# Optimization experiments

Measured on AMD Instinct MI355X. Metric: run time of the kernel, lower is better.

The kernel has to match this reference:

```python
import jax, jax.numpy as jnp
import numpy as np

N_NODES = 100000
N_EDGES = 1600000
IN_CH = 128
HEADS = 4
HID = 32
OUT_CH = 128
NEG_SLOPE = 0.2


def setup_inputs() -> dict:
    key = jax.random.key(0)
    ks = jax.random.split(key, 7)
    sc = 1.0 / np.sqrt(IN_CH)
    return {
        "x": jax.random.normal(ks[0], (N_NODES, IN_CH), dtype=jnp.float32),
        "edge_index": jax.random.randint(ks[1], (2, N_EDGES), 0, N_NODES, dtype=jnp.int32),
        "W": jax.random.normal(ks[2], (IN_CH, HEADS * HID), dtype=jnp.float32) * sc,
        "att_src": jax.random.normal(ks[3], (HEADS, HID), dtype=jnp.float32) * sc,
        "att_dst": jax.random.normal(ks[4], (HEADS, HID), dtype=jnp.float32) * sc,
        "lin_w": jax.random.normal(ks[5], (HEADS * HID, OUT_CH), dtype=jnp.float32) * (1.0 / np.sqrt(HEADS * HID)),
        "lin_b": jax.random.normal(ks[6], (OUT_CH,), dtype=jnp.float32) * 0.01,
    }


def reference(x, edge_index, W, att_src, att_dst, lin_w, lin_b):
    N = x.shape[0]
    src, dst = edge_index[0], edge_index[1]
    # node-wise linear transform -> [N, H, C]
    h = (x @ W).reshape(N, HEADS, HID)
    # per-node attention logit components [N, H]
    a_src = jnp.einsum("nhc,hc->nh", h, att_src)
    a_dst = jnp.einsum("nhc,hc->nh", h, att_dst)
    # per-edge logits with LeakyReLU [E, H]
    e = jax.nn.leaky_relu(a_src[src] + a_dst[dst], negative_slope=NEG_SLOPE)
    # segment softmax over destination neighborhoods
    m = jax.ops.segment_max(e, dst, num_segments=N)
    ex = jnp.exp(e - m[dst])
    s = jax.ops.segment_sum(ex, dst, num_segments=N)
    alpha = ex / (s[dst] + 1e-16)
    # weighted scatter-sum of source features [N, H, C] -> concat heads
    msg = h[src] * alpha[:, :, None]
    out = jax.ops.segment_sum(msg, dst, num_segments=N).reshape(N, HEADS * HID)
    # trailing dense + ReLU
    return jax.nn.relu(out @ lin_w + lin_b)
```

## Files before the change

kernel.cpp:

```cpp
#include <hip/hip_runtime.h>
#include <hip/hip_fp16.h>

#define NB   256
#define NBLK 256
#define BSH  9

typedef _Float16 f16;
typedef _Float16 half8 __attribute__((ext_vector_type(8)));
typedef __fp16 pk16x2 __attribute__((ext_vector_type(2)));
typedef float f32x4 __attribute__((ext_vector_type(4)));

__global__ void k_prep(const float* __restrict__ W, const float* __restrict__ LW,
                       f16* __restrict__ Wt, f16* __restrict__ LWt)
{
    int n = blockIdx.x & 127;
    const float* src = (blockIdx.x < 128) ? W : LW;
    f16* dst = (blockIdx.x < 128) ? Wt : LWt;
    int k = threadIdx.x;
    dst[n * 128 + k] = (f16)src[k * 128 + n];
}

__global__ __launch_bounds__(256) void k_gemm_att(
    const float* __restrict__ A, const f16* __restrict__ Wt,
    const float* __restrict__ att_s, const float* __restrict__ att_d,
    f16* __restrict__ Hh, float* __restrict__ as_out, float* __restrict__ ad_out,
    int M)
{
    __shared__ __align__(16) f16 as_lds[64 * 136];
    int t = threadIdx.x;
    int row0 = blockIdx.x * 64;

    {
        int r = t >> 2, kq = (t & 3) * 32;
        const float* ap = A + (size_t)(row0 + r) * 128 + kq;
        bool valid = (row0 + r) < M;
        pk16x2 hb[16];
#pragma unroll
        for (int j = 0; j < 8; ++j) {
            float4 v = valid ? *(const float4*)(ap + j * 4) : make_float4(0.f, 0.f, 0.f, 0.f);
            hb[2 * j]     = __builtin_amdgcn_cvt_pkrtz(v.x, v.y);
            hb[2 * j + 1] = __builtin_amdgcn_cvt_pkrtz(v.z, v.w);
        }
        f16* dst = as_lds + r * 136 + kq;
#pragma unroll
        for (int j = 0; j < 4; ++j) *(float4*)(dst + j * 8) = ((float4*)hb)[j];
    }
    __syncthreads();

    int w = t >> 6, ln = t & 63;
    int rr = (w & 1) * 32;
    int cc = (w >> 1) * 64;
    int q = ln >> 4, m = ln & 15;

    f32x4 acc[2][4];
#pragma unroll
    for (int i = 0; i < 2; ++i)
#pragma unroll
        for (int j = 0; j < 4; ++j) acc[i][j] = (f32x4){0.f, 0.f, 0.f, 0.f};

    const f16* wp = Wt + (size_t)(cc + m) * 128 + q * 8;
#pragma unroll
    for (int ks = 0; ks < 4; ++ks) {
        int k0 = ks * 32 + q * 8;
        half8 a0 = *(const half8*)(as_lds + (rr + m) * 136 + k0);
        half8 a1 = *(const half8*)(as_lds + (rr + 16 + m) * 136 + k0);
        half8 bf[4];
#pragma unroll
        for (int j = 0; j < 4; ++j)
            bf[j] = *(const half8*)(wp + j * 16 * 128 + ks * 32);
#pragma unroll
        for (int j = 0; j < 4; ++j) {
            acc[0][j] = __builtin_amdgcn_mfma_f32_16x16x32_f16(a0, bf[j], acc[0][j], 0, 0, 0);
            acc[1][j] = __builtin_amdgcn_mfma_f32_16x16x32_f16(a1, bf[j], acc[1][j], 0, 0, 0);
        }
    }
    __syncthreads();
#pragma unroll
    for (int i = 0; i < 2; ++i)
#pragma unroll
        for (int j = 0; j < 4; ++j)
#pragma unroll
            for (int g = 0; g < 4; ++g)
                as_lds[(rr + i * 16 + q * 4 + g) * 136 + cc + j * 16 + m] = (f16)acc[i][j][g];
    __syncthreads();
    {
        int r = t >> 2, cq = (t & 3) * 32;
        if (row0 + r < M) {
            float4 o0 = *(const float4*)(as_lds + r * 136 + cq);
            float4 o1 = *(const float4*)(as_lds + r * 136 + cq + 8);
            float4 o2 = *(const float4*)(as_lds + r * 136 + cq + 16);
            float4 o3 = *(const float4*)(as_lds + r * 136 + cq + 24);
            float4* hp = (float4*)(Hh + (size_t)(row0 + r) * 128 + cq);
            hp[0] = o0; hp[1] = o1; hp[2] = o2; hp[3] = o3;
        }
    }
    {
        int rl = w * 16 + m;
        int head = q;
        float ds = 0.f, dd = 0.f;
#pragma unroll
        for (int ch = 0; ch < 4; ++ch) {
            half8 hv = *(const half8*)(as_lds + rl * 136 + head * 32 + ch * 8);
            float4 s0 = *(const float4*)(att_s + head * 32 + ch * 8);
            float4 s1 = *(const float4*)(att_s + head * 32 + ch * 8 + 4);
            float4 d0 = *(const float4*)(att_d + head * 32 + ch * 8);
            float4 d1 = *(const float4*)(att_d + head * 32 + ch * 8 + 4);
            ds += (float)hv[0] * s0.x + (float)hv[1] * s0.y + (float)hv[2] * s0.z + (float)hv[3] * s0.w
                + (float)hv[4] * s1.x + (float)hv[5] * s1.y + (float)hv[6] * s1.z + (float)hv[7] * s1.w;
            dd += (float)hv[0] * d0.x + (float)hv[1] * d0.y + (float)hv[2] * d0.z + (float)hv[3] * d0.w
                + (float)hv[4] * d1.x + (float)hv[5] * d1.y + (float)hv[6] * d1.z + (float)hv[7] * d1.w;
        }
        if (row0 + rl < M) {
            as_out[(row0 + rl) * 4 + head] = ds;
            ad_out[(row0 + rl) * 4 + head] = dd;
        }
    }
}

__global__ __launch_bounds__(256) void k_gemm_bias_relu(
    const f16* __restrict__ Ah, const f16* __restrict__ LWt,
    const float* __restrict__ bias, float* __restrict__ Out, int M)
{
    __shared__ __align__(16) f16 as_lds[64 * 136];
    int t = threadIdx.x;
    int row0 = blockIdx.x * 64;
    {
        int r = t >> 2, kq = (t & 3) * 32;
        f16* dst = as_lds + r * 136 + kq;
        if (row0 + r < M) {
            const float4* ap = (const float4*)(Ah + (size_t)(row0 + r) * 128 + kq);
#pragma unroll
            for (int j = 0; j < 4; ++j) *(float4*)(dst + j * 8) = ap[j];
        } else {
            float4 z = make_float4(0.f, 0.f, 0.f, 0.f);
#pragma unroll
            for (int j = 0; j < 4; ++j) *(float4*)(dst + j * 8) = z;
        }
    }
    __syncthreads();

    int w = t >> 6, ln = t & 63;
    int rr = (w & 1) * 32;
    int cc = (w >> 1) * 64;
    int q = ln >> 4, m = ln & 15;

    f32x4 acc[2][4];
#pragma unroll
    for (int i = 0; i < 2; ++i)
#pragma unroll
        for (int j = 0; j < 4; ++j) acc[i][j] = (f32x4){0.f, 0.f, 0.f, 0.f};

    const f16* wp = LWt + (size_t)(cc + m) * 128 + q * 8;
#pragma unroll
    for (int ks = 0; ks < 4; ++ks) {
        int k0 = ks * 32 + q * 8;
        half8 a0 = *(const half8*)(as_lds + (rr + m) * 136 + k0);
        half8 a1 = *(const half8*)(as_lds + (rr + 16 + m) * 136 + k0);
        half8 bf[4];
#pragma unroll
        for (int j = 0; j < 4; ++j)
            bf[j] = *(const half8*)(wp + j * 16 * 128 + ks * 32);
#pragma unroll
        for (int j = 0; j < 4; ++j) {
            acc[0][j] = __builtin_amdgcn_mfma_f32_16x16x32_f16(a0, bf[j], acc[0][j], 0, 0, 0);
            acc[1][j] = __builtin_amdgcn_mfma_f32_16x16x32_f16(a1, bf[j], acc[1][j], 0, 0, 0);
        }
    }
    float bv[4];
#pragma unroll
    for (int j = 0; j < 4; ++j) bv[j] = bias[cc + j * 16 + m];
#pragma unroll
    for (int i = 0; i < 2; ++i)
#pragma unroll
        for (int g = 0; g < 4; ++g) {
            int row = row0 + rr + i * 16 + q * 4 + g;
            if (row < M) {
#pragma unroll
                for (int j = 0; j < 4; ++j)
                    Out[(size_t)row * 128 + cc + j * 16 + m] = fmaxf(acc[i][j][g] + bv[j], 0.f);
            }
        }
}


__global__ __launch_bounds__(256) void k_ph_hist(
    const int* __restrict__ dst, int* __restrict__ bh, int E, int chunk)
{
    __shared__ int hist[NB];
    int t = threadIdx.x;
    hist[t] = 0;
    __syncthreads();
    int e0 = blockIdx.x * chunk;
    int e1 = min(e0 + chunk, E);
    for (int e = e0 + t; e < e1; e += 256)
        atomicAdd(&hist[dst[e] >> BSH], 1);
    __syncthreads();
    bh[t * NBLK + blockIdx.x] = hist[t];
}

__global__ __launch_bounds__(1024) void k_ph_scan(int* __restrict__ bh)
{
    __shared__ int sd[1024];
    const int per = (NB * NBLK) / 1024;
    int t = threadIdx.x;
    int base = t * per;
    int loc[per];
    int sum = 0;
#pragma unroll
    for (int j = 0; j < per; ++j) { loc[j] = bh[base + j]; sum += loc[j]; }
    sd[t] = sum;
    __syncthreads();
    for (int o = 1; o < 1024; o <<= 1) {
        int x = (t >= o) ? sd[t - o] : 0;
        __syncthreads();
        sd[t] += x;
        __syncthreads();
    }
    int run = sd[t] - sum;
#pragma unroll
    for (int j = 0; j < per; ++j) { bh[base + j] = run; run += loc[j]; }
}

__global__ __launch_bounds__(256) void k_ph_bin(
    const int* __restrict__ ei, const int* __restrict__ bh,
    int* __restrict__ binned, int E, int chunk)
{
    __shared__ int boff[NB];
    int t = threadIdx.x;
    boff[t] = bh[t * NBLK + blockIdx.x];
    __syncthreads();
    int e0 = blockIdx.x * chunk;
    int e1 = min(e0 + chunk, E);
    for (int e = e0 + t; e < e1; e += 256) {
        int s = ei[e];
        int d = ei[E + e];
        int p = atomicAdd(&boff[d >> BSH], 1);
        binned[p] = s | ((d & ((1 << BSH) - 1)) << 17);
    }
}

__global__ __launch_bounds__(256) void k_ph_csr(
    const int* __restrict__ binned, const int* __restrict__ bh,
    int* __restrict__ csr, int* __restrict__ off, int* __restrict__ deg,
    int N, int E)
{
    __shared__ int cnt[512], loff[512], sd[256];
    int b = blockIdx.x;
    int lo = b << BSH;
    if (lo >= N) return;
    int t = threadIdx.x;
    int seg = bh[b * NBLK];
    int segend = (b + 1 < NB) ? bh[(b + 1) * NBLK] : E;
    int len = segend - seg;
    cnt[t] = 0; cnt[t + 256] = 0;
    __syncthreads();
    for (int i = t; i < len; i += 256)
        atomicAdd(&cnt[(unsigned)binned[seg + i] >> 17], 1);
    __syncthreads();
    int a0 = cnt[2 * t], a1 = cnt[2 * t + 1];
    int s = a0 + a1;
    sd[t] = s;
    __syncthreads();
    for (int o = 1; o < 256; o <<= 1) {
        int x = (t >= o) ? sd[t - o] : 0;
        __syncthreads();
        sd[t] += x;
        __syncthreads();
    }
    int ex = sd[t] - s;
    loff[2 * t] = ex;
    loff[2 * t + 1] = ex + a0;
    int n0 = lo + 2 * t;
    if (n0 < N)     { off[n0] = seg + ex;          deg[n0] = a0; }
    if (n0 + 1 < N) { off[n0 + 1] = seg + ex + a0; deg[n0 + 1] = a1; }
    __syncthreads();
    for (int i = t; i < len; i += 256) {
        int v = binned[seg + i];
        int p = atomicAdd(&loff[(unsigned)v >> 17], 1);
        csr[seg + p] = v & 0x1ffff;
    }
}

__global__ __launch_bounds__(256) void k_gather(
    const __half* __restrict__ Hh, const float* __restrict__ as_,
    const float* __restrict__ ad_, const int* __restrict__ off,
    const int* __restrict__ deg, const int* __restrict__ csr,
    __half* __restrict__ P, int N)
{
    __shared__ __half2 exh[4][4][68];
    __shared__ int src_s[4][64];
    int wid = threadIdx.x >> 6;
    int lane = threadIdx.x & 63;
    int n = blockIdx.x * 4 + wid;
    if (n >= N) return;
    int dg = deg[n];
    int base = off[n];
    float4 adn = *(const float4*)(ad_ + (size_t)n * 4);
    int g = lane >> 4;
    int li = lane & 15;
    int hh = li >> 2;
    float s0 = 0.f, s1 = 0.f, s2 = 0.f, s3 = 0.f;
    float acc[8] = {0.f, 0.f, 0.f, 0.f, 0.f, 0.f, 0.f, 0.f};

    for (int c0 = 0; c0 < dg; c0 += 64) {
        int cnt = min(64, dg - c0);
        {
            int idx = c0 + lane;
            int se = csr[base + min(idx, dg - 1)];
            float4 as = *(const float4*)(as_ + (size_t)se * 4);
            float e0 = as.x + adn.x, e1 = as.y + adn.y;
            float e2 = as.z + adn.z, e3 = as.w + adn.w;
            e0 = fmaxf(e0, 0.2f * e0); e1 = fmaxf(e1, 0.2f * e1);
            e2 = fmaxf(e2, 0.2f * e2); e3 = fmaxf(e3, 0.2f * e3);
            float x0 = __expf(e0), x1 = __expf(e1);
            float x2 = __expf(e2), x3 = __expf(e3);
            if (idx >= dg) { x0 = x1 = x2 = x3 = 0.f; }
            s0 += x0; s1 += x1; s2 += x2; s3 += x3;
            exh[wid][0][lane] = __float2half2_rn(x0);
            exh[wid][1][lane] = __float2half2_rn(x1);
            exh[wid][2][lane] = __float2half2_rn(x2);
            exh[wid][3][lane] = __float2half2_rn(x3);
            src_s[wid][lane] = se;
        }
        __asm__ volatile("s_waitcnt lgkmcnt(0)" ::: "memory");
        int iters = (cnt + 3) >> 2;
        __half2 ah[4];
        ah[0] = ah[1] = ah[2] = ah[3] = __float2half2_rn(0.f);
        for (int ii = 0; ii < iters; ++ii) {
            int j = ii * 4 + g;
            __half2 w2 = exh[wid][hh][j];
            int se = src_s[wid][j];
            float4 raw = *(const float4*)(Hh + (size_t)se * 128 + li * 8);
            __half2* ph = (__half2*)&raw;
            ah[0] = __hfma2(ph[0], w2, ah[0]);
            ah[1] = __hfma2(ph[1], w2, ah[1]);
            ah[2] = __hfma2(ph[2], w2, ah[2]);
            ah[3] = __hfma2(ph[3], w2, ah[3]);
            if ((ii & 7) == 7) {
#pragma unroll
                for (int k = 0; k < 4; ++k) {
                    float2 f = __half22float2(ah[k]);
                    acc[2 * k] += f.x; acc[2 * k + 1] += f.y;
                    ah[k] = __float2half2_rn(0.f);
                }
            }
        }
#pragma unroll
        for (int k = 0; k < 4; ++k) {
            float2 f = __half22float2(ah[k]);
            acc[2 * k] += f.x; acc[2 * k + 1] += f.y;
        }
        __asm__ volatile("s_waitcnt lgkmcnt(0)" ::: "memory");
    }

#pragma unroll
    for (int o = 1; o < 64; o <<= 1) {
        s0 += __shfl_xor(s0, o);
        s1 += __shfl_xor(s1, o);
        s2 += __shfl_xor(s2, o);
        s3 += __shfl_xor(s3, o);
    }
#pragma unroll
    for (int o = 16; o < 64; o <<= 1)
#pragma unroll
        for (int c = 0; c < 8; ++c) acc[c] += __shfl_xor(acc[c], o);

    float sh = (hh == 0) ? s0 : (hh == 1) ? s1 : (hh == 2) ? s2 : s3;
    float inv = 1.f / (sh + 1e-16f);
    if (g == 0) {
        __half2 o4[4];
#pragma unroll
        for (int k = 0; k < 4; ++k)
            o4[k] = __float22half2_rn(make_float2(acc[2 * k] * inv, acc[2 * k + 1] * inv));
        *(float4*)(P + (size_t)n * 128 + li * 8) = *(float4*)o4;
    }
}


extern "C" void kernel_launch(void* const* d_in, const int* in_sizes, int n_in,
                              void* d_out, int out_size, void* d_ws, size_t ws_size,
                              hipStream_t stream)
{
    const float* x     = (const float*)d_in[0];
    const int*   ei    = (const int*)d_in[1];
    const float* W     = (const float*)d_in[2];
    const float* att_s = (const float*)d_in[3];
    const float* att_d = (const float*)d_in[4];
    const float* lin_w = (const float*)d_in[5];
    const float* lin_b = (const float*)d_in[6];
    float* out = (float*)d_out;
    int N = in_sizes[0] / 128;
    int E = in_sizes[1] / 2;

    char* p = (char*)d_ws;
    auto alloc = [&](size_t bytes) { char* r = p; p += (bytes + 255) & ~(size_t)255; return r; };
    f16*    Hh   = (f16*)alloc((size_t)N * 128 * 2);
    f16*    P    = (f16*)alloc((size_t)N * 128 * 2);
    f16*    Wt   = (f16*)alloc(128 * 128 * 2);
    f16*    LWt  = (f16*)alloc(128 * 128 * 2);
    float*  AS   = (float*)alloc((size_t)N * 4 * 4);
    float*  AD   = (float*)alloc((size_t)N * 4 * 4);
    int*    deg  = (int*)alloc((size_t)N * 4);
    int*    off  = (int*)alloc((size_t)N * 4);
    int*    csr  = (int*)alloc((size_t)E * 4);
    int*    binned = (int*)alloc((size_t)E * 4);
    int*    bh   = (int*)alloc((size_t)NB * NBLK * 4);

    int chunk = (E + NBLK - 1) / NBLK;
    int mb = (N + 63) / 64;
    k_prep<<<256, 128, 0, stream>>>(W, lin_w, Wt, LWt);
    k_gemm_att<<<mb, 256, 0, stream>>>(x, Wt, att_s, att_d, Hh, AS, AD, N);
    k_ph_hist<<<NBLK, 256, 0, stream>>>(ei + E, bh, E, chunk);
    k_ph_scan<<<1, 1024, 0, stream>>>(bh);
    k_ph_bin<<<NBLK, 256, 0, stream>>>(ei, bh, binned, E, chunk);
    k_ph_csr<<<NB, 256, 0, stream>>>(binned, bh, csr, off, deg, N, E);
    k_gather<<<(N + 3) / 4, 256, 0, stream>>>((const __half*)Hh, AS, AD, off, deg, csr, (__half*)P, N);
    k_gemm_bias_relu<<<mb, 256, 0, stream>>>(P, LWt, lin_b, out, N);
}
```

Baseline: 303.9 us.

## Fuse neighbor aggregation with output GEMM through shared memory

The gather-aggregate kernel and the trailing dense+bias+ReLU GEMM are merged into one kernel. Each block of four waves aggregates 64 destination nodes, 16 per wave, into an LDS tile, then runs the MFMA GEMM on that tile directly. This removes the global round trip of the intermediate P buffer and one kernel launch. The edge weight and source index are also packed into one int2 LDS entry. The cost is 16x fewer blocks with a serial per-wave node loop, so occupancy and load balance over uneven degrees get worse.

```diff
diff --git a/kernel.cpp b/kernel.cpp
--- a/kernel.cpp
+++ b/kernel.cpp
@@ -117,71 +117,6 @@
     }
 }
 
-__global__ __launch_bounds__(256) void k_gemm_bias_relu(
-    const f16* __restrict__ Ah, const f16* __restrict__ LWt,
-    const float* __restrict__ bias, float* __restrict__ Out, int M)
-{
-    __shared__ __align__(16) f16 as_lds[64 * 136];
-    int t = threadIdx.x;
-    int row0 = blockIdx.x * 64;
-    {
-        int r = t >> 2, kq = (t & 3) * 32;
-        f16* dst = as_lds + r * 136 + kq;
-        if (row0 + r < M) {
-            const float4* ap = (const float4*)(Ah + (size_t)(row0 + r) * 128 + kq);
-#pragma unroll
-            for (int j = 0; j < 4; ++j) *(float4*)(dst + j * 8) = ap[j];
-        } else {
-            float4 z = make_float4(0.f, 0.f, 0.f, 0.f);
-#pragma unroll
-            for (int j = 0; j < 4; ++j) *(float4*)(dst + j * 8) = z;
-        }
-    }
-    __syncthreads();
-
-    int w = t >> 6, ln = t & 63;
-    int rr = (w & 1) * 32;
-    int cc = (w >> 1) * 64;
-    int q = ln >> 4, m = ln & 15;
-
-    f32x4 acc[2][4];
-#pragma unroll
-    for (int i = 0; i < 2; ++i)
-#pragma unroll
-        for (int j = 0; j < 4; ++j) acc[i][j] = (f32x4){0.f, 0.f, 0.f, 0.f};
-
-    const f16* wp = LWt + (size_t)(cc + m) * 128 + q * 8;
-#pragma unroll
-    for (int ks = 0; ks < 4; ++ks) {
-        int k0 = ks * 32 + q * 8;
-        half8 a0 = *(const half8*)(as_lds + (rr + m) * 136 + k0);
-        half8 a1 = *(const half8*)(as_lds + (rr + 16 + m) * 136 + k0);
-        half8 bf[4];
-#pragma unroll
-        for (int j = 0; j < 4; ++j)
-            bf[j] = *(const half8*)(wp + j * 16 * 128 + ks * 32);
-#pragma unroll
-        for (int j = 0; j < 4; ++j) {
-            acc[0][j] = __builtin_amdgcn_mfma_f32_16x16x32_f16(a0, bf[j], acc[0][j], 0, 0, 0);
-            acc[1][j] = __builtin_amdgcn_mfma_f32_16x16x32_f16(a1, bf[j], acc[1][j], 0, 0, 0);
-        }
-    }
-    float bv[4];
-#pragma unroll
-    for (int j = 0; j < 4; ++j) bv[j] = bias[cc + j * 16 + m];
-#pragma unroll
-    for (int i = 0; i < 2; ++i)
-#pragma unroll
-        for (int g = 0; g < 4; ++g) {
-            int row = row0 + rr + i * 16 + q * 4 + g;
-            if (row < M) {
-#pragma unroll
-                for (int j = 0; j < 4; ++j)
-                    Out[(size_t)row * 128 + cc + j * 16 + m] = fmaxf(acc[i][j][g] + bv[j], 0.f);
-            }
-        }
-}
-
 
 __global__ __launch_bounds__(256) void k_ph_hist(
     const int* __restrict__ dst, int* __restrict__ bh, int E, int chunk)
@@ -281,99 +216,149 @@
     }
 }
 
-__global__ __launch_bounds__(256) void k_gather(
+__global__ __launch_bounds__(256) void k_gather_gemm(
     const __half* __restrict__ Hh, const float* __restrict__ as_,
     const float* __restrict__ ad_, const int* __restrict__ off,
     const int* __restrict__ deg, const int* __restrict__ csr,
-    __half* __restrict__ P, int N)
-{
-    __shared__ __half2 exh[4][4][68];
-    __shared__ int src_s[4][64];
-    int wid = threadIdx.x >> 6;
-    int lane = threadIdx.x & 63;
-    int n = blockIdx.x * 4 + wid;
-    if (n >= N) return;
-    int dg = deg[n];
-    int base = off[n];
-    float4 adn = *(const float4*)(ad_ + (size_t)n * 4);
+    const f16* __restrict__ LWt, const float* __restrict__ bias,
+    float* __restrict__ Out, int N)
+{
+    __shared__ __align__(16) f16 p_lds[64 * 136];
+    __shared__ int2 ews[4][4][68];
+    int t = threadIdx.x;
+    int w = t >> 6, lane = t & 63;
+    int row0 = blockIdx.x * 64;
+
     int g = lane >> 4;
     int li = lane & 15;
     int hh = li >> 2;
-    float s0 = 0.f, s1 = 0.f, s2 = 0.f, s3 = 0.f;
-    float acc[8] = {0.f, 0.f, 0.f, 0.f, 0.f, 0.f, 0.f, 0.f};
-
-    for (int c0 = 0; c0 < dg; c0 += 64) {
-        int cnt = min(64, dg - c0);
-        {
-            int idx = c0 + lane;
-            int se = csr[base + min(idx, dg - 1)];
-            float4 as = *(const float4*)(as_ + (size_t)se * 4);
-            float e0 = as.x + adn.x, e1 = as.y + adn.y;
-            float e2 = as.z + adn.z, e3 = as.w + adn.w;
-            e0 = fmaxf(e0, 0.2f * e0); e1 = fmaxf(e1, 0.2f * e1);
-            e2 = fmaxf(e2, 0.2f * e2); e3 = fmaxf(e3, 0.2f * e3);
-            float x0 = __expf(e0), x1 = __expf(e1);
-            float x2 = __expf(e2), x3 = __expf(e3);
-            if (idx >= dg) { x0 = x1 = x2 = x3 = 0.f; }
-            s0 += x0; s1 += x1; s2 += x2; s3 += x3;
-            exh[wid][0][lane] = __float2half2_rn(x0);
-            exh[wid][1][lane] = __float2half2_rn(x1);
-            exh[wid][2][lane] = __float2half2_rn(x2);
-            exh[wid][3][lane] = __float2half2_rn(x3);
-            src_s[wid][lane] = se;
-        }
-        __asm__ volatile("s_waitcnt lgkmcnt(0)" ::: "memory");
-        int iters = (cnt + 3) >> 2;
-        __half2 ah[4];
-        ah[0] = ah[1] = ah[2] = ah[3] = __float2half2_rn(0.f);
-        for (int ii = 0; ii < iters; ++ii) {
-            int j = ii * 4 + g;
-            __half2 w2 = exh[wid][hh][j];
-            int se = src_s[wid][j];
-            float4 raw = *(const float4*)(Hh + (size_t)se * 128 + li * 8);
-            __half2* ph = (__half2*)&raw;
-            ah[0] = __hfma2(ph[0], w2, ah[0]);
-            ah[1] = __hfma2(ph[1], w2, ah[1]);
-            ah[2] = __hfma2(ph[2], w2, ah[2]);
-            ah[3] = __hfma2(ph[3], w2, ah[3]);
-            if ((ii & 7) == 7) {
-#pragma unroll
-                for (int k = 0; k < 4; ++k) {
-                    float2 f = __half22float2(ah[k]);
-                    acc[2 * k] += f.x; acc[2 * k + 1] += f.y;
-                    ah[k] = __float2half2_rn(0.f);
+
+    for (int nl = 0; nl < 16; ++nl) {
+        int ln = w * 16 + nl;
+        int n = row0 + ln;
+        if (n >= N) break;
+        int dg = deg[n];
+        int base = off[n];
+        float4 adn = *(const float4*)(ad_ + (size_t)n * 4);
+        float s0 = 0.f, s1 = 0.f, s2 = 0.f, s3 = 0.f;
+        float acc[8] = {0.f, 0.f, 0.f, 0.f, 0.f, 0.f, 0.f, 0.f};
+
+        for (int c0 = 0; c0 < dg; c0 += 64) {
+            int cnt = min(64, dg - c0);
+            {
+                int idx = c0 + lane;
+                int se = csr[base + min(idx, dg - 1)];
+                float4 as = *(const float4*)(as_ + (size_t)se * 4);
+                float e0 = as.x + adn.x, e1 = as.y + adn.y;
+                float e2 = as.z + adn.z, e3 = as.w + adn.w;
+                e0 = fmaxf(e0, 0.2f * e0); e1 = fmaxf(e1, 0.2f * e1);
+                e2 = fmaxf(e2, 0.2f * e2); e3 = fmaxf(e3, 0.2f * e3);
+                float x0 = __expf(e0), x1 = __expf(e1);
+                float x2 = __expf(e2), x3 = __expf(e3);
+                if (idx >= dg) { x0 = x1 = x2 = x3 = 0.f; }
+                s0 += x0; s1 += x1; s2 += x2; s3 += x3;
+                __half2 w0 = __float2half2_rn(x0), w1 = __float2half2_rn(x1);
+                __half2 w2h = __float2half2_rn(x2), w3 = __float2half2_rn(x3);
+                ews[w][0][lane] = make_int2(*(int*)&w0, se);
+                ews[w][1][lane] = make_int2(*(int*)&w1, se);
+                ews[w][2][lane] = make_int2(*(int*)&w2h, se);
+                ews[w][3][lane] = make_int2(*(int*)&w3, se);
+            }
+            __asm__ volatile("s_waitcnt lgkmcnt(0)" ::: "memory");
+            int iters = (cnt + 3) >> 2;
+            __half2 ah[4];
+            ah[0] = ah[1] = ah[2] = ah[3] = __float2half2_rn(0.f);
+            for (int ii = 0; ii < iters; ++ii) {
+                int j = ii * 4 + g;
+                int2 e = ews[w][hh][j];
+                __half2 w2 = *(__half2*)&e.x;
+                float4 raw = *(const float4*)(Hh + (size_t)e.y * 128 + li * 8);
+                __half2* ph = (__half2*)&raw;
+                ah[0] = __hfma2(ph[0], w2, ah[0]);
+                ah[1] = __hfma2(ph[1], w2, ah[1]);
+                ah[2] = __hfma2(ph[2], w2, ah[2]);
+                ah[3] = __hfma2(ph[3], w2, ah[3]);
+                if ((ii & 7) == 7) {
+#pragma unroll
+                    for (int k = 0; k < 4; ++k) {
+                        float2 f = __half22float2(ah[k]);
+                        acc[2 * k] += f.x; acc[2 * k + 1] += f.y;
+                        ah[k] = __float2half2_rn(0.f);
+                    }
                 }
             }
-        }
-#pragma unroll
-        for (int k = 0; k < 4; ++k) {
-            float2 f = __half22float2(ah[k]);
-            acc[2 * k] += f.x; acc[2 * k + 1] += f.y;
-        }
-        __asm__ volatile("s_waitcnt lgkmcnt(0)" ::: "memory");
-    }
-
-#pragma unroll
-    for (int o = 1; o < 64; o <<= 1) {
-        s0 += __shfl_xor(s0, o);
-        s1 += __shfl_xor(s1, o);
-        s2 += __shfl_xor(s2, o);
-        s3 += __shfl_xor(s3, o);
-    }
-#pragma unroll
-    for (int o = 16; o < 64; o <<= 1)
-#pragma unroll
-        for (int c = 0; c < 8; ++c) acc[c] += __shfl_xor(acc[c], o);
-
-    float sh = (hh == 0) ? s0 : (hh == 1) ? s1 : (hh == 2) ? s2 : s3;
-    float inv = 1.f / (sh + 1e-16f);
-    if (g == 0) {
-        __half2 o4[4];
-#pragma unroll
-        for (int k = 0; k < 4; ++k)
-            o4[k] = __float22half2_rn(make_float2(acc[2 * k] * inv, acc[2 * k + 1] * inv));
-        *(float4*)(P + (size_t)n * 128 + li * 8) = *(float4*)o4;
-    }
+#pragma unroll
+            for (int k = 0; k < 4; ++k) {
+                float2 f = __half22float2(ah[k]);
+                acc[2 * k] += f.x; acc[2 * k + 1] += f.y;
+            }
+            __asm__ volatile("s_waitcnt lgkmcnt(0)" ::: "memory");
+        }
+
+#pragma unroll
+        for (int o = 1; o < 64; o <<= 1) {
+            s0 += __shfl_xor(s0, o);
+            s1 += __shfl_xor(s1, o);
+            s2 += __shfl_xor(s2, o);
+            s3 += __shfl_xor(s3, o);
+        }
+#pragma unroll
+        for (int o = 16; o < 64; o <<= 1)
+#pragma unroll
+            for (int c = 0; c < 8; ++c) acc[c] += __shfl_xor(acc[c], o);
+
+        float sh = (hh == 0) ? s0 : (hh == 1) ? s1 : (hh == 2) ? s2 : s3;
+        float inv = 1.f / (sh + 1e-16f);
+        if (g == 0) {
+            pk16x2 o4[4];
+#pragma unroll
+            for (int k = 0; k < 4; ++k)
+                o4[k] = __builtin_amdgcn_cvt_pkrtz(acc[2 * k] * inv, acc[2 * k + 1] * inv);
+            *(float4*)(p_lds + ln * 136 + li * 8) = *(float4*)o4;
+        }
+    }
+    __syncthreads();
+
+    int rr = (w & 1) * 32;
+    int cc = (w >> 1) * 64;
+    int q = lane >> 4, m = lane & 15;
+
+    f32x4 gacc[2][4];
+#pragma unroll
+    for (int i = 0; i < 2; ++i)
+#pragma unroll
+        for (int j = 0; j < 4; ++j) gacc[i][j] = (f32x4){0.f, 0.f, 0.f, 0.f};
+
+    const f16* wp = LWt + (size_t)(cc + m) * 128 + q * 8;
+#pragma unroll
+    for (int ks = 0; ks < 4; ++ks) {
+        int k0 = ks * 32 + q * 8;
+        half8 a0 = *(const half8*)(p_lds + (rr + m) * 136 + k0);
+        half8 a1 = *(const half8*)(p_lds + (rr + 16 + m) * 136 + k0);
+        half8 bf[4];
+#pragma unroll
+        for (int j = 0; j < 4; ++j)
+            bf[j] = *(const half8*)(wp + j * 16 * 128 + ks * 32);
+#pragma unroll
+        for (int j = 0; j < 4; ++j) {
+            gacc[0][j] = __builtin_amdgcn_mfma_f32_16x16x32_f16(a0, bf[j], gacc[0][j], 0, 0, 0);
+            gacc[1][j] = __builtin_amdgcn_mfma_f32_16x16x32_f16(a1, bf[j], gacc[1][j], 0, 0, 0);
+        }
+    }
+    float bv[4];
+#pragma unroll
+    for (int j = 0; j < 4; ++j) bv[j] = bias[cc + j * 16 + m];
+#pragma unroll
+    for (int i = 0; i < 2; ++i)
+#pragma unroll
+        for (int g2 = 0; g2 < 4; ++g2) {
+            int row = row0 + rr + i * 16 + q * 4 + g2;
+            if (row < N) {
+#pragma unroll
+                for (int j = 0; j < 4; ++j)
+                    Out[(size_t)row * 128 + cc + j * 16 + m] = fmaxf(gacc[i][j][g2] + bv[j], 0.f);
+            }
+        }
 }
 
 
@@ -395,7 +380,6 @@
     char* p = (char*)d_ws;
     auto alloc = [&](size_t bytes) { char* r = p; p += (bytes + 255) & ~(size_t)255; return r; };
     f16*    Hh   = (f16*)alloc((size_t)N * 128 * 2);
-    f16*    P    = (f16*)alloc((size_t)N * 128 * 2);
     f16*    Wt   = (f16*)alloc(128 * 128 * 2);
     f16*    LWt  = (f16*)alloc(128 * 128 * 2);
     float*  AS   = (float*)alloc((size_t)N * 4 * 4);
@@ -414,6 +398,6 @@
     k_ph_scan<<<1, 1024, 0, stream>>>(bh);
     k_ph_bin<<<NBLK, 256, 0, stream>>>(ei, bh, binned, E, chunk);
     k_ph_csr<<<NB, 256, 0, stream>>>(binned, bh, csr, off, deg, N, E);
-    k_gather<<<(N + 3) / 4, 256, 0, stream>>>((const __half*)Hh, AS, AD, off, deg, csr, (__half*)P, N);
-    k_gemm_bias_relu<<<mb, 256, 0, stream>>>(P, LWt, lin_b, out, N);
-}
+    k_gather_gemm<<<mb, 256, 0, stream>>>((const __half*)Hh, AS, AD, off, deg, csr,
+                                          LWt, lin_b, out, N);
+}
```

Result: slower. 346.7 us (+14.1%).

## Fuse CSR build stages into one persistent kernel with grid barriers

Applied to the files above, without the earlier changes.

Merges weight transpose, histogram, scan, binning and per-bucket CSR construction into a single 256-block kernel separated by software grid barriers on global atomics. The single-block 1024-thread scan becomes a two-level parallel scan spread across all blocks. The aim is to remove several launch gaps and the serial scan kernel. It depends on all 256 blocks being co-resident and adds a memset launch to reset the barrier counters.

```diff
diff --git a/kernel.cpp b/kernel.cpp
--- a/kernel.cpp
+++ b/kernel.cpp
@@ -10,14 +10,110 @@
 typedef __fp16 pk16x2 __attribute__((ext_vector_type(2)));
 typedef float f32x4 __attribute__((ext_vector_type(4)));
 
-__global__ void k_prep(const float* __restrict__ W, const float* __restrict__ LW,
-                       f16* __restrict__ Wt, f16* __restrict__ LWt)
-{
-    int n = blockIdx.x & 127;
-    const float* src = (blockIdx.x < 128) ? W : LW;
-    f16* dst = (blockIdx.x < 128) ? Wt : LWt;
-    int k = threadIdx.x;
-    dst[n * 128 + k] = (f16)src[k * 128 + n];
+__device__ __forceinline__ void gridbar(int* bar, int idx, int nb)
+{
+    __syncthreads();
+    if (threadIdx.x == 0) {
+        __threadfence();
+        __hip_atomic_fetch_add(&bar[idx], 1, __ATOMIC_ACQ_REL, __HIP_MEMORY_SCOPE_AGENT);
+        while (__hip_atomic_load(&bar[idx], __ATOMIC_ACQUIRE, __HIP_MEMORY_SCOPE_AGENT) < nb)
+            __builtin_amdgcn_s_sleep(8);
+    }
+    __syncthreads();
+}
+
+__global__ __launch_bounds__(256) void k_csr_build(
+    const int* __restrict__ ei, const float* __restrict__ Wf,
+    const float* __restrict__ LWf, f16* __restrict__ Wt, f16* __restrict__ LWt,
+    int* __restrict__ bh, int* __restrict__ bsum, int* __restrict__ binned,
+    int* __restrict__ csr, int* __restrict__ off, int* __restrict__ deg,
+    int* __restrict__ bar, int N, int E, int chunk)
+{
+    __shared__ int sh[512];
+    __shared__ int sh2[512];
+    int t = threadIdx.x;
+    int b = blockIdx.x;
+    int e0 = b * chunk, e1 = min(e0 + chunk, E);
+
+    if (b < 128) {
+        if (t < 128) Wt[b * 128 + t] = (f16)Wf[t * 128 + b];
+        else         LWt[b * 128 + (t - 128)] = (f16)LWf[(t - 128) * 128 + b];
+    }
+    sh[t] = 0;
+    __syncthreads();
+    for (int e = e0 + t; e < e1; e += 256)
+        atomicAdd(&sh[ei[E + e] >> BSH], 1);
+    __syncthreads();
+    bh[t * NBLK + b] = sh[t];
+    gridbar(bar, 0, NBLK);
+
+    {
+        int v = bh[b * 256 + t];
+        sh[t] = v;
+        __syncthreads();
+        for (int o = 1; o < 256; o <<= 1) {
+            int x = (t >= o) ? sh[t - o] : 0;
+            __syncthreads(); sh[t] += x; __syncthreads();
+        }
+        int excl = sh[t] - v;
+        sh2[t] = excl;
+        if (t == 255) bsum[b] = sh[255];
+        gridbar(bar, 1, NBLK);
+        int bv = (t < b) ? bsum[t] : 0;
+        sh[t] = bv;
+        __syncthreads();
+        for (int o = 1; o < 256; o <<= 1) {
+            int x = (t >= o) ? sh[t - o] : 0;
+            __syncthreads(); sh[t] += x; __syncthreads();
+        }
+        bh[b * 256 + t] = sh[255] + sh2[t];
+    }
+    gridbar(bar, 2, NBLK);
+
+    {
+        sh[t] = bh[t * NBLK + b];
+        __syncthreads();
+        for (int e = e0 + t; e < e1; e += 256) {
+            int s = ei[e];
+            int d = ei[E + e];
+            int p = atomicAdd(&sh[d >> BSH], 1);
+            binned[p] = s | ((d & ((1 << BSH) - 1)) << 17);
+        }
+    }
+    gridbar(bar, 3, NBLK);
+
+    {
+        int lo = b << BSH;
+        int seg = bh[b * NBLK];
+        int segend = (b + 1 < NB) ? bh[(b + 1) * NBLK] : E;
+        int len = segend - seg;
+        sh[t] = 0; sh[t + 256] = 0;
+        __syncthreads();
+        for (int i = t; i < len; i += 256)
+            atomicAdd(&sh[(unsigned)binned[seg + i] >> 17], 1);
+        __syncthreads();
+        int a0 = sh[2 * t], a1 = sh[2 * t + 1];
+        int s = a0 + a1;
+        __syncthreads();
+        sh[t] = s;
+        __syncthreads();
+        for (int o = 1; o < 256; o <<= 1) {
+            int x = (t >= o) ? sh[t - o] : 0;
+            __syncthreads(); sh[t] += x; __syncthreads();
+        }
+        int ex = sh[t] - s;
+        sh2[2 * t] = ex;
+        sh2[2 * t + 1] = ex + a0;
+        int n0 = lo + 2 * t;
+        if (n0 < N)     { off[n0] = seg + ex;          deg[n0] = a0; }
+        if (n0 + 1 < N) { off[n0 + 1] = seg + ex + a0; deg[n0 + 1] = a1; }
+        __syncthreads();
+        for (int i = t; i < len; i += 256) {
+            int v = binned[seg + i];
+            int p = atomicAdd(&sh2[(unsigned)v >> 17], 1);
+            csr[seg + p] = v & 0x1ffff;
+        }
+    }
 }
 
 __global__ __launch_bounds__(256) void k_gemm_att(
@@ -180,105 +276,6 @@
                     Out[(size_t)row * 128 + cc + j * 16 + m] = fmaxf(acc[i][j][g] + bv[j], 0.f);
             }
         }
-}
-
-
-__global__ __launch_bounds__(256) void k_ph_hist(
-    const int* __restrict__ dst, int* __restrict__ bh, int E, int chunk)
-{
-    __shared__ int hist[NB];
-    int t = threadIdx.x;
-    hist[t] = 0;
-    __syncthreads();
-    int e0 = blockIdx.x * chunk;
-    int e1 = min(e0 + chunk, E);
-    for (int e = e0 + t; e < e1; e += 256)
-        atomicAdd(&hist[dst[e] >> BSH], 1);
-    __syncthreads();
-    bh[t * NBLK + blockIdx.x] = hist[t];
-}
-
-__global__ __launch_bounds__(1024) void k_ph_scan(int* __restrict__ bh)
-{
-    __shared__ int sd[1024];
-    const int per = (NB * NBLK) / 1024;
-    int t = threadIdx.x;
-    int base = t * per;
-    int loc[per];
-    int sum = 0;
-#pragma unroll
-    for (int j = 0; j < per; ++j) { loc[j] = bh[base + j]; sum += loc[j]; }
-    sd[t] = sum;
-    __syncthreads();
-    for (int o = 1; o < 1024; o <<= 1) {
-        int x = (t >= o) ? sd[t - o] : 0;
-        __syncthreads();
-        sd[t] += x;
-        __syncthreads();
-    }
-    int run = sd[t] - sum;
-#pragma unroll
-    for (int j = 0; j < per; ++j) { bh[base + j] = run; run += loc[j]; }
-}
-
-__global__ __launch_bounds__(256) void k_ph_bin(
-    const int* __restrict__ ei, const int* __restrict__ bh,
-    int* __restrict__ binned, int E, int chunk)
-{
-    __shared__ int boff[NB];
-    int t = threadIdx.x;
-    boff[t] = bh[t * NBLK + blockIdx.x];
-    __syncthreads();
-    int e0 = blockIdx.x * chunk;
-    int e1 = min(e0 + chunk, E);
-    for (int e = e0 + t; e < e1; e += 256) {
-        int s = ei[e];
-        int d = ei[E + e];
-        int p = atomicAdd(&boff[d >> BSH], 1);
-        binned[p] = s | ((d & ((1 << BSH) - 1)) << 17);
-    }
-}
-
-__global__ __launch_bounds__(256) void k_ph_csr(
-    const int* __restrict__ binned, const int* __restrict__ bh,
-    int* __restrict__ csr, int* __restrict__ off, int* __restrict__ deg,
-    int N, int E)
-{
-    __shared__ int cnt[512], loff[512], sd[256];
-    int b = blockIdx.x;
-    int lo = b << BSH;
-    if (lo >= N) return;
-    int t = threadIdx.x;
-    int seg = bh[b * NBLK];
-    int segend = (b + 1 < NB) ? bh[(b + 1) * NBLK] : E;
-    int len = segend - seg;
-    cnt[t] = 0; cnt[t + 256] = 0;
-    __syncthreads();
-    for (int i = t; i < len; i += 256)
-        atomicAdd(&cnt[(unsigned)binned[seg + i] >> 17], 1);
-    __syncthreads();
-    int a0 = cnt[2 * t], a1 = cnt[2 * t + 1];
-    int s = a0 + a1;
-    sd[t] = s;
-    __syncthreads();
-    for (int o = 1; o < 256; o <<= 1) {
-        int x = (t >= o) ? sd[t - o] : 0;
-        __syncthreads();
-        sd[t] += x;
-        __syncthreads();
-    }
-    int ex = sd[t] - s;
-    loff[2 * t] = ex;
-    loff[2 * t + 1] = ex + a0;
-    int n0 = lo + 2 * t;
-    if (n0 < N)     { off[n0] = seg + ex;          deg[n0] = a0; }
-    if (n0 + 1 < N) { off[n0 + 1] = seg + ex + a0; deg[n0 + 1] = a1; }
-    __syncthreads();
-    for (int i = t; i < len; i += 256) {
-        int v = binned[seg + i];
-        int p = atomicAdd(&loff[(unsigned)v >> 17], 1);
-        csr[seg + p] = v & 0x1ffff;
-    }
 }
 
 __global__ __launch_bounds__(256) void k_gather(
@@ -394,26 +391,28 @@
 
     char* p = (char*)d_ws;
     auto alloc = [&](size_t bytes) { char* r = p; p += (bytes + 255) & ~(size_t)255; return r; };
-    f16*    Hh   = (f16*)alloc((size_t)N * 128 * 2);
-    f16*    P    = (f16*)alloc((size_t)N * 128 * 2);
-    f16*    Wt   = (f16*)alloc(128 * 128 * 2);
-    f16*    LWt  = (f16*)alloc(128 * 128 * 2);
-    float*  AS   = (float*)alloc((size_t)N * 4 * 4);
-    float*  AD   = (float*)alloc((size_t)N * 4 * 4);
-    int*    deg  = (int*)alloc((size_t)N * 4);
-    int*    off  = (int*)alloc((size_t)N * 4);
-    int*    csr  = (int*)alloc((size_t)E * 4);
+    f16*    Hh     = (f16*)alloc((size_t)N * 128 * 2);
+    f16*    P      = (f16*)alloc((size_t)N * 128 * 2);
+    f16*    Wt     = (f16*)alloc(128 * 128 * 2);
+    f16*    LWt    = (f16*)alloc(128 * 128 * 2);
+    float*  AS     = (float*)alloc((size_t)N * 4 * 4);
+    float*  AD     = (float*)alloc((size_t)N * 4 * 4);
+    int*    deg    = (int*)alloc((size_t)N * 4);
+    int*    off    = (int*)alloc((size_t)N * 4);
+    int*    csr    = (int*)alloc((size_t)E * 4);
     int*    binned = (int*)alloc((size_t)E * 4);
-    int*    bh   = (int*)alloc((size_t)NB * NBLK * 4);
+    int*    bh     = (int*)alloc((size_t)NB * NBLK * 4);
+    int*    bsum   = (int*)alloc(NBLK * 4);
+    int*    bar    = (int*)alloc(256);
 
     int chunk = (E + NBLK - 1) / NBLK;
     int mb = (N + 63) / 64;
-    k_prep<<<256, 128, 0, stream>>>(W, lin_w, Wt, LWt);
+
+    hipMemsetAsync(bar, 0, 256, stream);
+    k_csr_build<<<NBLK, 256, 0, stream>>>(ei, W, lin_w, Wt, LWt, bh, bsum,
+                                          binned, csr, off, deg, bar, N, E, chunk);
     k_gemm_att<<<mb, 256, 0, stream>>>(x, Wt, att_s, att_d, Hh, AS, AD, N);
-    k_ph_hist<<<NBLK, 256, 0, stream>>>(ei + E, bh, E, chunk);
-    k_ph_scan<<<1, 1024, 0, stream>>>(bh);
-    k_ph_bin<<<NBLK, 256, 0, stream>>>(ei, bh, binned, E, chunk);
-    k_ph_csr<<<NB, 256, 0, stream>>>(binned, bh, csr, off, deg, N, E);
-    k_gather<<<(N + 3) / 4, 256, 0, stream>>>((const __half*)Hh, AS, AD, off, deg, csr, (__half*)P, N);
+    k_gather<<<(N + 3) / 4, 256, 0, stream>>>((const __half*)Hh, AS, AD, off, deg, csr,
+                                              (__half*)P, N);
     k_gemm_bias_relu<<<mb, 256, 0, stream>>>(P, LWt, lin_b, out, N);
 }
```

Result: slower. 400.0 us (+31.6%).
